# Kernel tuning notes

Hardware: AMD Instinct MI355X
Metric: run time of the kernel (lower is better)

The kernel has to match this reference:

```python
import jax, jax.numpy as jnp
import numpy as np

NT, NE = 2, 2            # node types, edge types
N, FIN, HID = 50000, 128, 128
H, D, L, E = 4, 32, 2, 400000
EDGE_SRC = (0, 1)        # edge type e: src node type
EDGE_DST = (1, 0)        # edge type e: dst node type


def _segment_softmax(scores, seg, n):
    # scores: [E, H], softmax over edges sharing the same dst node
    m = jax.ops.segment_max(scores, seg, num_segments=n)
    e = jnp.exp(scores - m[seg])
    s = jax.ops.segment_sum(e, seg, num_segments=n)
    return e / (s[seg] + 1e-16)


def setup_inputs() -> dict:
    key = jax.random.key(0)
    ks = iter(jax.random.split(key, 40))
    rn = lambda shape, sc=1.0: jax.random.normal(next(ks), shape, dtype=jnp.float32) * sc
    s_in, s_h, s_d = 1.0 / np.sqrt(FIN), 1.0 / np.sqrt(HID), 1.0 / np.sqrt(D)
    inp = {}
    inp["x"] = rn((NT, N, FIN))
    inp["ei"] = jax.random.randint(next(ks), (NE, 2, E), 0, N, dtype=jnp.int32)
    inp["ew"] = rn((NE, E))
    inp["lin_w"] = rn((NT, FIN, HID), s_in)
    inp["lin_b"] = jnp.zeros((NT, HID), jnp.float32)
    for nm in ("k", "q", "v", "a"):
        inp[nm + "_w"] = rn((L, NT, HID, HID), s_h)
        inp[nm + "_b"] = jnp.zeros((L, NT, HID), jnp.float32)
    inp["skip"] = jnp.ones((L, NT), jnp.float32)
    inp["rel_att"] = rn((L, NE, H, D, D), s_d)
    inp["rel_msg"] = rn((L, NE, H, D, D), s_d)
    inp["rel_p"] = jnp.ones((L, NE, H), jnp.float32)
    return inp


def reference(x, ei, ew, lin_w, lin_b, k_w, k_b, q_w, q_b, v_w, v_b,
              a_w, a_b, skip, rel_att, rel_msg, rel_p):
    inv_sqrt_d = jnp.float32(1.0 / np.sqrt(D))
    # per-node-type input projection + ReLU
    h = jax.nn.relu(jnp.einsum('tnf,tfh->tnh', x, lin_w) + lin_b[:, None, :])
    # sigmoid edge-weight scaling of source rows (last-write on duplicates, as torch *=)
    w = jax.nn.sigmoid(ew)  # [NE, E]
    for e in range(NE):
        s = EDGE_SRC[e]
        src = ei[e, 0]
        h = h.at[s, src].set(h[s, src] * w[e][:, None])
    for l in range(L):
        k = (jnp.einsum('tnh,tho->tno', h, k_w[l]) + k_b[l][:, None, :]).reshape(NT, N, H, D)
        q = (jnp.einsum('tnh,tho->tno', h, q_w[l]) + q_b[l][:, None, :]).reshape(NT, N, H, D)
        v = (jnp.einsum('tnh,tho->tno', h, v_w[l]) + v_b[l][:, None, :]).reshape(NT, N, H, D)
        agg = jnp.zeros((NT, N, H, D), h.dtype)
        for e in range(NE):
            s, t = EDGE_SRC[e], EDGE_DST[e]
            src, dst = ei[e, 0], ei[e, 1]
            k_rel = jnp.einsum('nhd,hde->nhe', k[s], rel_att[l, e])  # [N, H, D]
            v_rel = jnp.einsum('nhd,hde->nhe', v[s], rel_msg[l, e])
            alpha = jnp.einsum('ehd,ehd->eh', q[t][dst], k_rel[src]) * rel_p[l, e] * inv_sqrt_d
            alpha = _segment_softmax(alpha, dst, N)                  # [E, H]
            msg = v_rel[src] * alpha[:, :, None]                     # [E, H, D]
            agg = agg.at[t].add(jax.ops.segment_sum(msg, dst, num_segments=N))
        out = jnp.einsum('tnh,tho->tno', jax.nn.gelu(agg.reshape(NT, N, HID), approximate=False), a_w[l]) + a_b[l][:, None, :]
        beta = jax.nn.sigmoid(skip[l])[:, None, None]
        h = beta * out + (1.0 - beta) * h
    return h
```

## Files before the change

kernel.cpp:

```cpp
#include <hip/hip_runtime.h>
#include <hip/hip_bf16.h>
#include <math.h>

typedef __hip_bfloat16 bf16;
typedef _Float16 f16;
typedef __attribute__((ext_vector_type(2))) _Float16 f16x2;
typedef __attribute__((ext_vector_type(8))) short bf16x8;
typedef __attribute__((ext_vector_type(4))) float f32x4;

#define NT 2
#define NE 2
#define NN 50000
#define HID 128
#define NH 4
#define DD 32
#define NL 2
#define NEDGE 400000
#define MBLK64 782
#define AGGB 12500
#define WPITCH 136
#define CB 196
#define CAP 4096
#define CHUNK 2048
#define NCH 196

__device__ __forceinline__ float b2f(bf16 v) { return __bfloat162float(v); }
__device__ __forceinline__ float toF(float v) { return v; }
__device__ __forceinline__ float toF(bf16 v) { return b2f(v); }
__device__ __forceinline__ float sigm(float x) { return 1.0f / (1.0f + __expf(-x)); }
__device__ __forceinline__ unsigned short f2bits(float f) {
    bf16 h = __float2bfloat16(f);
    unsigned short b; __builtin_memcpy(&b, &h, 2); return b;
}
__device__ __forceinline__ float bits2f(unsigned short b) {
    unsigned u = ((unsigned)b) << 16; float f; __builtin_memcpy(&f, &u, 4); return f;
}
__device__ __forceinline__ unsigned short f2hbits(float f) {
    f16 h = (f16)f;
    unsigned short b; __builtin_memcpy(&b, &h, 2); return b;
}

__device__ __forceinline__ float dot8_f16(const unsigned* kr, const f16x2 q[4], float init) {
    float p = init;
#pragma unroll
    for (int i = 0; i < 4; i++) {
        f16x2 kh; __builtin_memcpy(&kh, &kr[i], 4);
#if __has_builtin(__builtin_amdgcn_fdot2)
        p = __builtin_amdgcn_fdot2(q[i], kh, p, false);
#else
        p += (float)q[i].x * (float)kh.x + (float)q[i].y * (float)kh.y;
#endif
    }
    return p;
}

__global__ void detect_kernel(const void* __restrict__ x, int* __restrict__ flag) {
    int lane = threadIdx.x;
    const unsigned short* u = (const unsigned short*)x;
    int cnt = 0;
    for (int i = 0; i < 4; i++) {
        unsigned short w = u[lane * 4 + i];
        int e = (w >> 7) & 0xFF;
        if (e >= 110 && e <= 135) cnt++;
    }
    for (int off = 32; off > 0; off >>= 1) cnt += __shfl_xor(cnt, off, 64);
    if (lane == 0) *flag = (cnt > 200) ? 0 : 1;
}

__global__ void bucket1_kernel(const int* __restrict__ ei, int* __restrict__ gcd,
                               int* __restrict__ gcs, unsigned* __restrict__ bufd,
                               unsigned* __restrict__ bufs) {
    int blk = blockIdx.x;
    int e = blk / NCH, ch = blk % NCH;
    int tid = threadIdx.x;
    __shared__ int hd[CB], hs[CB], bd[CB], bs[CB];
    for (int i = tid; i < CB; i += 256) { hd[i] = 0; hs[i] = 0; }
    __syncthreads();
    const int* srcp = ei + (e * 2 + 0) * NEDGE;
    const int* dstp = ei + (e * 2 + 1) * NEDGE;
    int j0 = ch * CHUNK;
    int src[8], dst[8], rd[8], rs[8];
#pragma unroll
    for (int i = 0; i < 8; i++) {
        int j = j0 + i * 256 + tid;
        if (j < NEDGE) {
            src[i] = srcp[j]; dst[i] = dstp[j];
            rd[i] = atomicAdd(&hd[dst[i] >> 8], 1);
            rs[i] = atomicAdd(&hs[src[i] >> 8], 1);
        } else src[i] = -1;
    }
    __syncthreads();
    for (int i = tid; i < CB; i += 256) {
        bd[i] = hd[i] ? atomicAdd(&gcd[e * CB + i], hd[i]) : 0;
        bs[i] = hs[i] ? atomicAdd(&gcs[e * CB + i], hs[i]) : 0;
    }
    __syncthreads();
#pragma unroll
    for (int i = 0; i < 8; i++) {
        int j = j0 + i * 256 + tid;
        if (j < NEDGE) {
            int bn = dst[i] >> 8;
            int pd = bd[bn] + rd[i]; if (pd >= CAP) pd = CAP - 1;
            bufd[((size_t)e * CB + bn) * CAP + pd] =
                ((unsigned)(dst[i] & 255) << 24) | (unsigned)src[i];
            bn = src[i] >> 8;
            int ps = bs[bn] + rs[i]; if (ps >= CAP) ps = CAP - 1;
            bufs[((size_t)e * CB + bn) * CAP + ps] =
                ((unsigned)(src[i] & 255) << 19) | (unsigned)j;
        }
    }
}

__global__ void cscan_kernel(const int* __restrict__ gcd, int* __restrict__ coff,
                             int* __restrict__ offs) {
    int e = blockIdx.x;
    int tid = threadIdx.x;
    __shared__ int sb[256];
    int v = (tid < CB) ? gcd[e * CB + tid] : 0;
    sb[tid] = v; __syncthreads();
    for (int off = 1; off < 256; off <<= 1) {
        int a = (tid >= off) ? sb[tid - off] : 0;
        __syncthreads();
        sb[tid] += a;
        __syncthreads();
    }
    if (tid < CB) coff[e * (CB + 1) + tid] = sb[tid] - v;
    if (tid == CB - 1) coff[e * (CB + 1) + CB] = sb[tid];
    if (tid == 0) offs[e * (NN + 1) + NN] = NEDGE;
}

__global__ void fine_dst_kernel(const unsigned* __restrict__ bufd, const int* __restrict__ gcd,
                                const int* __restrict__ coff, int* __restrict__ offs,
                                int* __restrict__ srcb) {
    int blk = blockIdx.x;
    int e = blk / CB, bn = blk % CB;
    int tid = threadIdx.x;
    int cnt = gcd[e * CB + bn]; if (cnt > CAP) cnt = CAP;
    int base = coff[e * (CB + 1) + bn];
    const unsigned* b = bufd + ((size_t)e * CB + bn) * CAP;
    __shared__ int dc[256], ss[256];
    dc[tid] = 0; __syncthreads();
    for (int i = tid; i < cnt; i += 256) atomicAdd(&dc[b[i] >> 24], 1);
    __syncthreads();
    int v = dc[tid];
    ss[tid] = v; __syncthreads();
    for (int off = 1; off < 256; off <<= 1) {
        int a = (tid >= off) ? ss[tid - off] : 0;
        __syncthreads();
        ss[tid] += a;
        __syncthreads();
    }
    int excl = ss[tid] - v;
    int d = bn * 256 + tid;
    if (d < NN) offs[e * (NN + 1) + d] = base + excl;
    dc[tid] = excl;
    __syncthreads();
    for (int i = tid; i < cnt; i += 256) {
        unsigned w = b[i];
        int r = atomicAdd(&dc[w >> 24], 1);
        srcb[(size_t)e * NEDGE + base + r] = (int)(w & 0xFFFFFF);
    }
}

__global__ void fine_src_kernel(const unsigned* __restrict__ bufs, const int* __restrict__ gcs,
                                const void* __restrict__ ew, float* __restrict__ ewsc,
                                const int* __restrict__ flag) {
    int blk = blockIdx.x;
    int e = blk / CB, bn = blk % CB;
    int tid = threadIdx.x;
    int cnt = gcs[e * CB + bn]; if (cnt > CAP) cnt = CAP;
    const unsigned* b = bufs + ((size_t)e * CB + bn) * CAP;
    __shared__ int mx[256];
    mx[tid] = -1; __syncthreads();
    for (int i = tid; i < cnt; i += 256) {
        unsigned w = b[i];
        atomicMax(&mx[w >> 19], (int)(w & 0x7FFFF));
    }
    __syncthreads();
    int n = bn * 256 + tid;
    if (n < NN) {
        int mj = mx[tid];
        float v = 1.0f;
        if (mj >= 0)
            v = sigm(*flag ? ((const float*)ew)[(size_t)e * NEDGE + mj]
                           : b2f(((const bf16*)ew)[(size_t)e * NEDGE + mj]));
        ewsc[e * NN + n] = v;
    }
}

template <typename T>
__device__ __forceinline__ void prep_w_body(const T* lin_w, const T* k_w, const T* q_w,
                                            const T* v_w, const T* a_w, const T* rel_att,
                                            const T* rel_msg, unsigned short* wT) {
    int bid = blockIdx.x, tid = threadIdx.x;
    int mat = bid >> 6;
    int elem = (bid & 63) * 256 + tid;
    int n = elem >> 7, k = elem & 127;
    float v;
    if (mat < 2) {
        v = toF(lin_w[(size_t)mat * 16384 + k * 128 + n]);
    } else if (mat < 14) {
        int m2 = mat - 2, lt = m2 / 3, op = m2 % 3;
        if (op == 1) {
            v = toF(q_w[(size_t)lt * 16384 + k * 128 + n]);
        } else {
            const T* w = (op == 0 ? k_w : v_w) + (size_t)lt * 16384 + k * 128;
            const T* rl = (op == 0 ? rel_att : rel_msg) + (size_t)lt * 4096;
            int hh = n >> 5, jj = n & 31;
            float s = 0.f;
#pragma unroll 8
            for (int d = 0; d < 32; d++)
                s += toF(w[hh * 32 + d]) * toF(rl[(hh * 32 + d) * 32 + jj]);
            v = s;
        }
    } else {
        v = toF(a_w[(size_t)(mat - 14) * 16384 + k * 128 + n]);
    }
    wT[(size_t)mat * 16384 + n * 128 + k] = f2bits(v);
}
__global__ void prep_w_kernel(const void* lin_w, const void* k_w, const void* q_w,
                              const void* v_w, const void* a_w, const void* rel_att,
                              const void* rel_msg, unsigned short* wT, const int* flag) {
    if (*flag) prep_w_body<float>((const float*)lin_w, (const float*)k_w, (const float*)q_w,
                                  (const float*)v_w, (const float*)a_w, (const float*)rel_att,
                                  (const float*)rel_msg, wT);
    else       prep_w_body<bf16>((const bf16*)lin_w, (const bf16*)k_w, (const bf16*)q_w,
                                 (const bf16*)v_w, (const bf16*)a_w, (const bf16*)rel_att,
                                 (const bf16*)rel_msg, wT);
}

template <typename T>
__device__ __forceinline__ void prep_misc_body(const T* lin_b, const T* k_b, const T* q_b,
                                               const T* v_b, const T* a_b, const T* rel_att,
                                               const T* rel_msg, const T* rel_p, const T* skip,
                                               float* biasall, float* relpf, float* skipf) {
    int mat = blockIdx.x, n = threadIdx.x;
    float v;
    if (mat < 2) {
        v = toF(lin_b[mat * 128 + n]);
    } else if (mat < 14) {
        int m2 = mat - 2, lt = m2 / 3, op = m2 % 3;
        if (op == 1) {
            v = toF(q_b[lt * 128 + n]);
        } else {
            const T* b = (op == 0 ? k_b : v_b) + lt * 128;
            const T* rl = (op == 0 ? rel_att : rel_msg) + (size_t)lt * 4096;
            int hh = n >> 5, jj = n & 31;
            float s = 0.f;
#pragma unroll 8
            for (int d = 0; d < 32; d++)
                s += toF(b[hh * 32 + d]) * toF(rl[(hh * 32 + d) * 32 + jj]);
            v = s;
        }
    } else {
        v = toF(a_b[(mat - 14) * 128 + n]);
    }
    biasall[mat * 128 + n] = v;
    if (mat == 0 && n < 16) relpf[n] = toF(rel_p[n]);
    if (mat == 1 && n < 4) skipf[n] = toF(skip[n]);
}
__global__ void prep_misc_kernel(const void* lin_b, const void* k_b, const void* q_b,
                                 const void* v_b, const void* a_b, const void* rel_att,
                                 const void* rel_msg, const void* rel_p, const void* skip,
                                 float* biasall, float* relpf, float* skipf, const int* flag) {
    if (*flag) prep_misc_body<float>((const float*)lin_b, (const float*)k_b, (const float*)q_b,
                                     (const float*)v_b, (const float*)a_b, (const float*)rel_att,
                                     (const float*)rel_msg, (const float*)rel_p, (const float*)skip,
                                     biasall, relpf, skipf);
    else       prep_misc_body<bf16>((const bf16*)lin_b, (const bf16*)k_b, (const bf16*)q_b,
                                    (const bf16*)v_b, (const bf16*)a_b, (const bf16*)rel_att,
                                    (const bf16*)rel_msg, (const bf16*)rel_p, (const bf16*)skip,
                                    biasall, relpf, skipf);
}

__device__ __forceinline__ void stage_w(unsigned short* __restrict__ Wl,
                                        const unsigned short* __restrict__ wmat, int tid) {
#pragma unroll
    for (int i = 0; i < 8; i++) {
        int c = i * 256 + tid;
        int n = c >> 4, ko = (c & 15) * 8;
        *(bf16x8*)&Wl[n * WPITCH + ko] = *(const bf16x8*)&wmat[n * 128 + ko];
    }
}

__device__ __forceinline__ void mfma_pass(const unsigned short* __restrict__ Wl,
                                          const bf16x8 af[4], const float* __restrict__ bias,
                                          f32x4 acc[8], int m16, int quad) {
#pragma unroll
    for (int ni = 0; ni < 8; ni++) {
        float b = bias[ni * 16 + m16];
        f32x4 iv = {b, b, b, b};
        acc[ni] = iv;
    }
#pragma unroll
    for (int ks = 0; ks < 4; ks++) {
        bf16x8 a = af[ks];
#pragma unroll
        for (int ni = 0; ni < 8; ni++) {
            bf16x8 bb = *(const bf16x8*)&Wl[(ni * 16 + m16) * WPITCH + ks * 32 + quad * 8];
            acc[ni] = __builtin_amdgcn_mfma_f32_16x16x32_bf16(a, bb, acc[ni], 0, 0, 0);
        }
    }
}

template <bool FP32>
__device__ __forceinline__ void lin_body(const void* __restrict__ x,
                                         const unsigned short* __restrict__ wT,
                                         const float* __restrict__ biasall,
                                         const float* __restrict__ ewsc,
                                         float* __restrict__ h) {
    __shared__ unsigned short Wl[128 * WPITCH];
    int bid = blockIdx.x, tid = threadIdx.x;
    int t = bid / MBLK64, nb = (bid % MBLK64) * 64;
    int wave = tid >> 6, lane = tid & 63;
    int m16 = lane & 15, quad = lane >> 4;
    stage_w(Wl, wT + (size_t)t * 16384, tid);
    int arow = nb + wave * 16 + m16;
    int arc = arow < NN ? arow : NN - 1;
    size_t abase = ((size_t)t * NN + arc) * 128;
    bf16x8 af[4];
#pragma unroll
    for (int ks = 0; ks < 4; ks++) {
        if (FP32) {
            const float4* s = (const float4*)((const float*)x + abase + ks * 32 + quad * 8);
            float4 f0 = s[0], f1 = s[1];
            unsigned short* pu = (unsigned short*)&af[ks];
            pu[0] = f2bits(f0.x); pu[1] = f2bits(f0.y); pu[2] = f2bits(f0.z); pu[3] = f2bits(f0.w);
            pu[4] = f2bits(f1.x); pu[5] = f2bits(f1.y); pu[6] = f2bits(f1.z); pu[7] = f2bits(f1.w);
        } else {
            af[ks] = *(const bf16x8*)((const unsigned short*)x + abase + ks * 32 + quad * 8);
        }
    }
    __syncthreads();
    f32x4 acc[8];
    mfma_pass(Wl, af, biasall + t * 128, acc, m16, quad);
#pragma unroll
    for (int r = 0; r < 4; r++) {
        int node = nb + wave * 16 + quad * 4 + r;
        if (node < NN) {
            float es = ewsc[t * NN + node];
            size_t ro = ((size_t)t * NN + node) * 128;
#pragma unroll
            for (int ni = 0; ni < 8; ni++)
                h[ro + ni * 16 + m16] = fmaxf(acc[ni][r], 0.f) * es;
        }
    }
}
__global__ void __launch_bounds__(256, 4) lin_gemm(const void* x, const unsigned short* wT,
                                                   const float* biasall, const float* ewsc,
                                                   float* h, const int* flag) {
    if (*flag) lin_body<true>(x, wT, biasall, ewsc, h);
    else       lin_body<false>(x, wT, biasall, ewsc, h);
}

__global__ void __launch_bounds__(256, 4) kqv_gemm(const float* __restrict__ h,
                                                   const unsigned short* __restrict__ wTall,
                                                   const float* __restrict__ biasall, int l,
                                                   unsigned short* __restrict__ kk,
                                                   unsigned short* __restrict__ qq,
                                                   unsigned short* __restrict__ vv) {
    __shared__ unsigned short Wl[128 * WPITCH];
    int bid = blockIdx.x, tid = threadIdx.x;
    int t = bid / MBLK64, nb = (bid % MBLK64) * 64;
    int lt = l * 2 + t;
    int wave = tid >> 6, lane = tid & 63;
    int m16 = lane & 15, quad = lane >> 4;
    int arow = nb + wave * 16 + m16;
    int arc = arow < NN ? arow : NN - 1;
    size_t abase = ((size_t)t * NN + arc) * 128;
    bf16x8 af[4];
#pragma unroll
    for (int ks = 0; ks < 4; ks++) {
        const float4* s = (const float4*)(h + abase + ks * 32 + quad * 8);
        float4 f0 = s[0], f1 = s[1];
        unsigned short* pu = (unsigned short*)&af[ks];
        pu[0] = f2bits(f0.x); pu[1] = f2bits(f0.y); pu[2] = f2bits(f0.z); pu[3] = f2bits(f0.w);
        pu[4] = f2bits(f1.x); pu[5] = f2bits(f1.y); pu[6] = f2bits(f1.z); pu[7] = f2bits(f1.w);
    }
    f32x4 acc[8];
#pragma unroll
    for (int pass = 0; pass < 3; pass++) {
        int mat = 2 + lt * 3 + pass;
        __syncthreads();
        stage_w(Wl, wTall + (size_t)mat * 16384, tid);
        __syncthreads();
        mfma_pass(Wl, af, biasall + mat * 128, acc, m16, quad);
        unsigned short* dst = (pass == 0) ? kk : (pass == 1 ? qq : vv);
#pragma unroll
        for (int r = 0; r < 4; r++) {
            int node = nb + wave * 16 + quad * 4 + r;
            if (node < NN) {
                size_t ro = ((size_t)t * NN + node) * 128;
#pragma unroll
                for (int ni = 0; ni < 8; ni++)
                    dst[ro + ni * 16 + m16] = f2hbits(acc[ni][r]);
            }
        }
    }
}

__global__ void __launch_bounds__(256) agg_kernel(const unsigned short* __restrict__ qq,
                                                  const unsigned short* __restrict__ kk,
                                                  const unsigned short* __restrict__ vv,
                                                  const int* __restrict__ srcb,
                                                  const int* __restrict__ offs,
                                                  const float* __restrict__ relpf, int l,
                                                  unsigned short* __restrict__ aggb) {
    int bid = blockIdx.x;
    int e = bid / AGGB;
    int wave = threadIdx.x >> 6, lane = threadIdx.x & 63;
    int dst = (bid % AGGB) * 4 + wave;
    int t = 1 - e;
    int le = l * 2 + e;
    int stream = lane >> 4, l4 = lane & 15;
    int c0 = l4 * 8, head = l4 >> 2;
    const int* offs_e = offs + e * (NN + 1);
    const int* srcb_e = srcb + (size_t)e * NEDGE;
    int beg = offs_e[dst], end = offs_e[dst + 1];
    size_t rowo = ((size_t)t * NN + dst) * 128 + c0;
    float scale = relpf[le * 4 + head] * 0.17677669529663687f * 1.44269504088896f;
    uint4 qraw = *(const uint4*)&qq[rowo];
    f16x2 q[4];
    __builtin_memcpy(&q[0], &qraw.x, 4); __builtin_memcpy(&q[1], &qraw.y, 4);
    __builtin_memcpy(&q[2], &qraw.z, 4); __builtin_memcpy(&q[3], &qraw.w, 4);
    const unsigned short* kb = kk + (size_t)e * NN * 128;
    const unsigned short* vb = vv + (size_t)e * NN * 128;
    float lsum = 0.f;
    float acc[8] = {0.f, 0.f, 0.f, 0.f, 0.f, 0.f, 0.f, 0.f};
    for (int j = beg + stream; j < end; j += 4) {
        int src = srcb_e[j];
        size_t so = (size_t)src * 128 + c0;
        uint4 kraw = *(const uint4*)&kb[so];
        uint4 vraw = *(const uint4*)&vb[so];
        float p = dot8_f16((const unsigned*)&kraw, q, 0.f);
        p += __shfl_xor(p, 1, 64);
        p += __shfl_xor(p, 2, 64);
        float es = exp2f(p * scale);
        lsum += es;
        const unsigned* vr = (const unsigned*)&vraw;
#pragma unroll
        for (int i = 0; i < 4; i++) {
            f16x2 vh; __builtin_memcpy(&vh, &vr[i], 4);
            acc[i * 2]     += es * (float)vh.x;
            acc[i * 2 + 1] += es * (float)vh.y;
        }
    }
    lsum += __shfl_xor(lsum, 16, 64);
#pragma unroll
    for (int i = 0; i < 8; i++) acc[i] += __shfl_xor(acc[i], 16, 64);
    lsum += __shfl_xor(lsum, 32, 64);
#pragma unroll
    for (int i = 0; i < 8; i++) acc[i] += __shfl_xor(acc[i], 32, 64);
    if (stream == 0) {
        float inv = 1.0f / (lsum + 1e-16f);
        unsigned short o[8];
#pragma unroll
        for (int i = 0; i < 8; i++) o[i] = f2bits(acc[i] * inv);
        *(bf16x8*)&aggb[rowo] = *(bf16x8*)o;
    }
}

__global__ void __launch_bounds__(256, 4) outproj_gemm(const unsigned short* __restrict__ aggb,
                                                       const unsigned short* __restrict__ wTall,
                                                       const float* __restrict__ biasall,
                                                       const float* __restrict__ skipf, int l,
                                                       float* __restrict__ h, int last,
                                                       void* __restrict__ outp,
                                                       const int* __restrict__ flag) {
    __shared__ unsigned short Wl[128 * WPITCH];
    int bid = blockIdx.x, tid = threadIdx.x;
    int t = bid / MBLK64, nb = (bid % MBLK64) * 64;
    int lt = l * 2 + t;
    int wave = tid >> 6, lane = tid & 63;
    int m16 = lane & 15, quad = lane >> 4;
    int mat = 14 + lt;
    stage_w(Wl, wTall + (size_t)mat * 16384, tid);
    int arow = nb + wave * 16 + m16;
    int arc = arow < NN ? arow : NN - 1;
    size_t abase = ((size_t)t * NN + arc) * 128;
    bf16x8 af[4];
#pragma unroll
    for (int ks = 0; ks < 4; ks++) {
        bf16x8 raw = *(const bf16x8*)&aggb[abase + ks * 32 + quad * 8];
        const unsigned short* ru = (const unsigned short*)&raw;
        unsigned short* pu = (unsigned short*)&af[ks];
#pragma unroll
        for (int jj = 0; jj < 8; jj++) {
            float g = bits2f(ru[jj]);
            pu[jj] = f2bits(0.5f * g * (1.0f + erff(g * 0.70710678118654752f)));
        }
    }
    __syncthreads();
    f32x4 acc[8];
    mfma_pass(Wl, af, biasall + mat * 128, acc, m16, quad);
    float beta = sigm(skipf[lt]);
    int fl = *flag;
#pragma unroll
    for (int r = 0; r < 4; r++) {
        int node = nb + wave * 16 + quad * 4 + r;
        if (node < NN) {
            size_t ro = ((size_t)t * NN + node) * 128;
#pragma unroll
            for (int ni = 0; ni < 8; ni++) {
                size_t io = ro + ni * 16 + m16;
                float nv = beta * acc[ni][r] + (1.0f - beta) * h[io];
                h[io] = nv;
                if (last) {
                    if (fl) ((float*)outp)[io] = nv;
                    else    ((bf16*)outp)[io] = __float2bfloat16(nv);
                }
            }
        }
    }
}

extern "C" void kernel_launch(void* const* d_in, const int* in_sizes, int n_in,
                              void* d_out, int out_size, void* d_ws, size_t ws_size,
                              hipStream_t stream) {
    const void* x      = d_in[0];
    const int*  ei     = (const int*)d_in[1];
    const void* ew     = d_in[2];
    const void* lin_w  = d_in[3];
    const void* lin_b  = d_in[4];
    const void* k_w    = d_in[5];
    const void* k_b    = d_in[6];
    const void* q_w    = d_in[7];
    const void* q_b    = d_in[8];
    const void* v_w    = d_in[9];
    const void* v_b    = d_in[10];
    const void* a_w    = d_in[11];
    const void* a_b    = d_in[12];
    const void* skip   = d_in[13];
    const void* rel_att = d_in[14];
    const void* rel_msg = d_in[15];
    const void* rel_p  = d_in[16];

    char* p = (char*)d_ws;
    auto alloc = [&](size_t bytes) -> char* {
        char* r = p;
        p += (bytes + 255) & ~(size_t)255;
        return r;
    };
    int* flag     = (int*)alloc(sizeof(int));
    int* gcd      = (int*)alloc(sizeof(int) * NE * CB);
    int* gcs      = (int*)alloc(sizeof(int) * NE * CB);
    int* coff     = (int*)alloc(sizeof(int) * NE * (CB + 1));
    int* offs     = (int*)alloc(sizeof(int) * NE * (NN + 1));
    int* srcb     = (int*)alloc(sizeof(int) * NE * NEDGE);
    unsigned* bufd = (unsigned*)alloc(sizeof(unsigned) * NE * CB * CAP);
    unsigned* bufs = (unsigned*)alloc(sizeof(unsigned) * NE * CB * CAP);
    unsigned short* wTall = (unsigned short*)alloc(sizeof(short) * 18 * 16384);
    float* biasall = (float*)alloc(sizeof(float) * 18 * 128);
    float* relpf   = (float*)alloc(sizeof(float) * 16);
    float* skipf   = (float*)alloc(sizeof(float) * 4);
    float* ewsc    = (float*)alloc(sizeof(float) * NT * NN);
    float* h       = (float*)alloc(sizeof(float) * NT * NN * HID);
    unsigned short* qq = (unsigned short*)alloc(sizeof(short) * NT * NN * HID);
    unsigned short* kk = (unsigned short*)alloc(sizeof(short) * NT * NN * HID);
    unsigned short* vv = (unsigned short*)alloc(sizeof(short) * NT * NN * HID);
    unsigned short* aggb = qq;

    hipMemsetAsync(gcd, 0, sizeof(int) * NE * CB, stream);
    hipMemsetAsync(gcs, 0, sizeof(int) * NE * CB, stream);

    detect_kernel<<<1, 64, 0, stream>>>(x, flag);
    bucket1_kernel<<<NE * NCH, 256, 0, stream>>>(ei, gcd, gcs, bufd, bufs);
    cscan_kernel<<<NE, 256, 0, stream>>>(gcd, coff, offs);
    fine_dst_kernel<<<NE * CB, 256, 0, stream>>>(bufd, gcd, coff, offs, srcb);
    fine_src_kernel<<<NE * CB, 256, 0, stream>>>(bufs, gcs, ew, ewsc, flag);
    prep_w_kernel<<<18 * 64, 256, 0, stream>>>(lin_w, k_w, q_w, v_w, a_w, rel_att, rel_msg,
                                               wTall, flag);
    prep_misc_kernel<<<18, 128, 0, stream>>>(lin_b, k_b, q_b, v_b, a_b, rel_att, rel_msg,
                                             rel_p, skip, biasall, relpf, skipf, flag);

    lin_gemm<<<NT * MBLK64, 256, 0, stream>>>(x, wTall, biasall, ewsc, h, flag);

    for (int l = 0; l < NL; l++) {
        kqv_gemm<<<NT * MBLK64, 256, 0, stream>>>(h, wTall, biasall, l, kk, qq, vv);
        agg_kernel<<<NE * AGGB, 256, 0, stream>>>(qq, kk, vv, srcb, offs, relpf, l, aggb);
        outproj_gemm<<<NT * MBLK64, 256, 0, stream>>>(aggb, wTall, biasall, skipf, l, h,
                                                      (l == NL - 1) ? 1 : 0, d_out, flag);
    }
}
```

Measured before the change: 449.6 us.

## Assign one destination node per 16-lane group and batch four edge gathers

The aggregation kernel now maps each 16-lane group to its own destination node, so a block covers 16 nodes instead of 4, and the block count drops to match. Each group walks its node's edge list four edges at a time, issuing all four K/V gathers before computing, with clamped indices and zeroed weights for the tail. This removes the cross-stream shuffle reduction and raises memory-level parallelism per lane. In exchange, groups within a wave now diverge on unequal in-degrees, and tail iterations do wasted loads.

```diff
diff --git a/kernel.cpp b/kernel.cpp
--- a/kernel.cpp
+++ b/kernel.cpp
@@ -17,7 +17,7 @@
 #define NL 2
 #define NEDGE 400000
 #define MBLK64 782
-#define AGGB 12500
+#define AGGB 3125
 #define WPITCH 136
 #define CB 196
 #define CAP 4096
@@ -409,10 +409,10 @@
     int bid = blockIdx.x;
     int e = bid / AGGB;
     int wave = threadIdx.x >> 6, lane = threadIdx.x & 63;
-    int dst = (bid % AGGB) * 4 + wave;
+    int stream = lane >> 4, l4 = lane & 15;
+    int dst = (bid % AGGB) * 16 + wave * 4 + stream;
     int t = 1 - e;
     int le = l * 2 + e;
-    int stream = lane >> 4, l4 = lane & 15;
     int c0 = l4 * 8, head = l4 >> 2;
     const int* offs_e = offs + e * (NN + 1);
     const int* srcb_e = srcb + (size_t)e * NEDGE;
@@ -427,37 +427,42 @@
     const unsigned short* vb = vv + (size_t)e * NN * 128;
     float lsum = 0.f;
     float acc[8] = {0.f, 0.f, 0.f, 0.f, 0.f, 0.f, 0.f, 0.f};
-    for (int j = beg + stream; j < end; j += 4) {
-        int src = srcb_e[j];
-        size_t so = (size_t)src * 128 + c0;
-        uint4 kraw = *(const uint4*)&kb[so];
-        uint4 vraw = *(const uint4*)&vb[so];
-        float p = dot8_f16((const unsigned*)&kraw, q, 0.f);
-        p += __shfl_xor(p, 1, 64);
-        p += __shfl_xor(p, 2, 64);
-        float es = exp2f(p * scale);
-        lsum += es;
-        const unsigned* vr = (const unsigned*)&vraw;
+    int jmax = end - 1;
+    for (int j0 = beg; j0 < end; j0 += 4) {
+        int src[4];
 #pragma unroll
         for (int i = 0; i < 4; i++) {
-            f16x2 vh; __builtin_memcpy(&vh, &vr[i], 4);
-            acc[i * 2]     += es * (float)vh.x;
-            acc[i * 2 + 1] += es * (float)vh.y;
-        }
-    }
-    lsum += __shfl_xor(lsum, 16, 64);
-#pragma unroll
-    for (int i = 0; i < 8; i++) acc[i] += __shfl_xor(acc[i], 16, 64);
-    lsum += __shfl_xor(lsum, 32, 64);
-#pragma unroll
-    for (int i = 0; i < 8; i++) acc[i] += __shfl_xor(acc[i], 32, 64);
-    if (stream == 0) {
-        float inv = 1.0f / (lsum + 1e-16f);
-        unsigned short o[8];
-#pragma unroll
-        for (int i = 0; i < 8; i++) o[i] = f2bits(acc[i] * inv);
-        *(bf16x8*)&aggb[rowo] = *(bf16x8*)o;
-    }
+            int j = j0 + i;
+            src[i] = srcb_e[j <= jmax ? j : jmax];
+        }
+        uint4 kr[4], vr[4];
+#pragma unroll
+        for (int i = 0; i < 4; i++) {
+            size_t so = (size_t)src[i] * 128 + c0;
+            kr[i] = *(const uint4*)&kb[so];
+            vr[i] = *(const uint4*)&vb[so];
+        }
+#pragma unroll
+        for (int i = 0; i < 4; i++) {
+            float p = dot8_f16((const unsigned*)&kr[i], q, 0.f);
+            p += __shfl_xor(p, 1, 64);
+            p += __shfl_xor(p, 2, 64);
+            float es = (j0 + i <= jmax) ? exp2f(p * scale) : 0.f;
+            lsum += es;
+            const unsigned* vu = (const unsigned*)&vr[i];
+#pragma unroll
+            for (int k = 0; k < 4; k++) {
+                f16x2 vh; __builtin_memcpy(&vh, &vu[k], 4);
+                acc[k * 2]     += es * (float)vh.x;
+                acc[k * 2 + 1] += es * (float)vh.y;
+            }
+        }
+    }
+    float inv = 1.0f / (lsum + 1e-16f);
+    unsigned short o[8];
+#pragma unroll
+    for (int i = 0; i < 8; i++) o[i] = f2bits(acc[i] * inv);
+    *(bf16x8*)&aggb[rowo] = *(bf16x8*)o;
 }
 
 __global__ void __launch_bounds__(256, 4) outproj_gemm(const unsigned short* __restrict__ aggb,
```

After: 449.7 us. About the same (+0.0%).
